# Kernel optimization log

Hardware: AMD Instinct MI355X
Metric: run time of the kernel (lower is better)

Reference implementation:

```python
import jax, jax.numpy as jnp
import numpy as np

DIM = 768
HEADS = 12
HEAD_DIM = DIM // HEADS


def setup_inputs() -> dict:
    key = jax.random.key(0)
    ks = jax.random.split(key, 5)
    B, N = 2, 2048
    x = jax.random.normal(ks[0], (B, N, DIM), dtype=jnp.float32)
    s = 1.0 / np.sqrt(DIM)
    qkv_w = jax.random.normal(ks[1], (3 * DIM, DIM), dtype=jnp.float32) * s
    qkv_b = jnp.zeros((3 * DIM,), dtype=jnp.float32)
    proj_w = jax.random.normal(ks[2], (DIM, DIM), dtype=jnp.float32) * s
    proj_b = jnp.zeros((DIM,), dtype=jnp.float32)
    return {"x": x, "qkv_w": qkv_w, "qkv_b": qkv_b, "proj_w": proj_w, "proj_b": proj_b}


def reference(x, qkv_w, qkv_b, proj_w, proj_b):
    B, N, C = x.shape
    scale = HEAD_DIM ** -0.5
    qkv = x @ qkv_w.T + qkv_b                      # [B,N,3C]
    qkv = qkv.reshape(B, N, 3, HEADS, HEAD_DIM)
    q = qkv[:, :, 0].transpose(0, 2, 1, 3)         # [B,H,N,D]
    k = qkv[:, :, 1].transpose(0, 2, 1, 3)
    v = qkv[:, :, 2].transpose(0, 2, 1, 3)
    attn = jnp.einsum('bhnd,bhmd->bhnm', q, k) * scale
    attn = jax.nn.softmax(attn, axis=-1)
    out = jnp.einsum('bhnm,bhmd->bhnd', attn, v)   # [B,H,N,D]
    out = out.transpose(0, 2, 1, 3).reshape(B, N, C)
    return out @ proj_w.T + proj_b
```

## Files before the change

kernel.cpp:

```cpp
#include <hip/hip_runtime.h>
#include <hip/hip_bf16.h>

typedef __bf16 bf16x8 __attribute__((ext_vector_type(8)));
typedef float f32x4 __attribute__((ext_vector_type(4)));
typedef float f32x16 __attribute__((ext_vector_type(16)));

#define SEQ   2048
#define NHEAD 12
#define NBH   24
#define QSCALE 0.18033688011112042f

__device__ __forceinline__ unsigned short f2bf(float f) {
  unsigned int u = __builtin_bit_cast(unsigned int, f);
  u += 0x7FFFu + ((u >> 16) & 1u);
  return (unsigned short)(u >> 16);
}
__device__ __forceinline__ unsigned int packbf2_trunc(float lo, float hi) {
  return __builtin_amdgcn_perm(__builtin_bit_cast(unsigned int, hi),
                               __builtin_bit_cast(unsigned int, lo), 0x07060302u);
}

#define NX4  786432
#define NW14 442368
#define NW24 147456
__global__ __launch_bounds__(256) void cvt3_kernel(const float4* __restrict__ x,
                                                   const float4* __restrict__ w1,
                                                   const float4* __restrict__ w2,
                                                   ushort4* __restrict__ xo,
                                                   ushort4* __restrict__ w1o,
                                                   ushort4* __restrict__ w2o) {
  int i = blockIdx.x * 256 + threadIdx.x;
  const float4* s;
  ushort4* d;
  int j = i;
  if (i < NX4)               { s = x;  d = xo; }
  else if (i < NX4 + NW14)   { s = w1; d = w1o; j = i - NX4; }
  else                       { s = w2; d = w2o; j = i - (NX4 + NW14); }
  float4 v = s[j];
  ushort4 r;
  r.x = f2bf(v.x); r.y = f2bf(v.y); r.z = f2bf(v.z); r.w = f2bf(v.w);
  d[j] = r;
}

template <int BM, int BN, int MODE>
__global__ __launch_bounds__(256) void gemm_kernel(const unsigned short* __restrict__ X,
                                                   const unsigned short* __restrict__ W,
                                                   const float* __restrict__ bias,
                                                   unsigned short* __restrict__ Qb,
                                                   unsigned short* __restrict__ Kb,
                                                   unsigned short* __restrict__ Vtb,
                                                   float* __restrict__ Out) {
  constexpr int K = 768, BK = 64;
  constexpr int WM = BM / 2, WN = BN / 2;
  constexpr int MT = WM / 16, NT = WN / 16;
  __shared__ __align__(16) unsigned short Xs[BM * BK];
  __shared__ __align__(16) unsigned short Ws[BN * BK];

  const int tid = threadIdx.x;
  const int w = tid >> 6, lane = tid & 63, quad = lane >> 4, m16 = lane & 15;
  const int wm = w & 1, wn = w >> 1;
  const int row0 = blockIdx.y * BM, col0 = blockIdx.x * BN;

  f32x4 acc[MT][NT];
#pragma unroll
  for (int mt = 0; mt < MT; ++mt)
#pragma unroll
    for (int nt = 0; nt < NT; ++nt) acc[mt][nt] = (f32x4){0.f, 0.f, 0.f, 0.f};

  for (int k0 = 0; k0 < K; k0 += BK) {
    __syncthreads();
#pragma unroll
    for (int j = 0; j < BM / 32; ++j) {
      int e = tid + 256 * j, r = e >> 3, c8 = e & 7;
      uint4 v = *(const uint4*)(X + (size_t)(row0 + r) * 768 + k0 + c8 * 8);
      *(uint4*)(Xs + r * BK + ((c8 ^ (r & 7)) << 3)) = v;
    }
#pragma unroll
    for (int j = 0; j < BN / 32; ++j) {
      int e = tid + 256 * j, r = e >> 3, c8 = e & 7;
      uint4 v = *(const uint4*)(W + (size_t)(col0 + r) * 768 + k0 + c8 * 8);
      *(uint4*)(Ws + r * BK + ((c8 ^ (r & 7)) << 3)) = v;
    }
    __syncthreads();
#pragma unroll
    for (int ks = 0; ks < 2; ++ks) {
      const int sw = ((quad + 4 * ks) ^ (m16 & 7)) << 3;
      bf16x8 a[MT], b[NT];
#pragma unroll
      for (int mt = 0; mt < MT; ++mt)
        a[mt] = *(const bf16x8*)(Xs + (wm * WM + mt * 16 + m16) * BK + sw);
#pragma unroll
      for (int nt = 0; nt < NT; ++nt)
        b[nt] = *(const bf16x8*)(Ws + (wn * WN + nt * 16 + m16) * BK + sw);
#pragma unroll
      for (int mt = 0; mt < MT; ++mt)
#pragma unroll
        for (int nt = 0; nt < NT; ++nt)
          acc[mt][nt] = __builtin_amdgcn_mfma_f32_16x16x32_bf16(a[mt], b[nt], acc[mt][nt], 0, 0, 0);
    }
  }

#pragma unroll
  for (int mt = 0; mt < MT; ++mt) {
#pragma unroll
    for (int nt = 0; nt < NT; ++nt) {
      const int m0 = row0 + wm * WM + mt * 16 + quad * 4;
      const int c = col0 + wn * WN + nt * 16 + m16;
      const float bia = bias[c];
      f32x4 v = acc[mt][nt];
      if constexpr (MODE == 0) {
        const int bidx = m0 >> 11, ns = m0 & 2047;
        if (c < 1536) {
          unsigned short* dst;
          float sc;
          int cc;
          if (c < 768) { cc = c; dst = Qb; sc = QSCALE; }
          else         { cc = c - 768; dst = Kb; sc = 1.0f; }
          const int h = cc >> 6, d = cc & 63;
          unsigned short* p = dst + ((size_t)(bidx * NHEAD + h) * SEQ + ns) * 64 + d;
          p[0]   = f2bf((v[0] + bia) * sc);
          p[64]  = f2bf((v[1] + bia) * sc);
          p[128] = f2bf((v[2] + bia) * sc);
          p[192] = f2bf((v[3] + bia) * sc);
        } else {
          const int cc = c - 1536, h = cc >> 6, d = cc & 63;
          ushort4 pk;
          pk.x = f2bf(v[0] + bia); pk.y = f2bf(v[1] + bia);
          pk.z = f2bf(v[2] + bia); pk.w = f2bf(v[3] + bia);
          *(ushort4*)(Vtb + ((size_t)(bidx * NHEAD + h) * 64 + d) * SEQ + ns) = pk;
        }
      } else {
        float* o = Out + (size_t)m0 * 768 + c;
        o[0]       = v[0] + bia;
        o[768]     = v[1] + bia;
        o[2 * 768] = v[2] + bia;
        o[3 * 768] = v[3] + bia;
      }
    }
  }
}

#define VPAD 136
__global__ __launch_bounds__(256, 2) void attn_kernel(const unsigned short* __restrict__ Qb,
                                                      const unsigned short* __restrict__ Kb,
                                                      const unsigned short* __restrict__ Vtb,
                                                      unsigned short* __restrict__ Ab) {
  __shared__ __align__(16) unsigned short Ks[128 * 64];
  __shared__ __align__(16) unsigned short Vts[64 * VPAD];

  const int tid = threadIdx.x;
  const int w = tid >> 6, lane = tid & 63, hi = lane >> 5, l32 = lane & 31;
  const int bh = blockIdx.x % NBH, qt = blockIdx.x / NBH;
  const int bb = bh / NHEAD, h = bh % NHEAD;
  const int q0 = qt * 128 + w * 32;

  const unsigned short* Qp = Qb + (size_t)bh * SEQ * 64;
  const unsigned short* Kp = Kb + (size_t)bh * SEQ * 64;
  const unsigned short* Vp = Vtb + (size_t)bh * 64 * SEQ;

  bf16x8 qf[4];
#pragma unroll
  for (int dc = 0; dc < 4; ++dc)
    qf[dc] = *(const bf16x8*)(Qp + (size_t)(q0 + l32) * 64 + dc * 16 + hi * 8);

  f32x16 o[2] = {};
  float m_i = -3.0e38f, l_i = 0.f;

  for (int kt = 0; kt < 16; ++kt) {
    __syncthreads();
#pragma unroll
    for (int j = 0; j < 4; ++j) {
      int e = tid + 256 * j, r = e >> 3, c8 = e & 7;
      uint4 v = *(const uint4*)(Kp + (size_t)(kt * 128 + r) * 64 + c8 * 8);
      *(uint4*)(Ks + r * 64 + ((c8 ^ (r & 7)) << 3)) = v;
    }
#pragma unroll
    for (int j = 0; j < 4; ++j) {
      int e = tid + 256 * j, d = e >> 4, c8 = e & 15;
      uint4 v = *(const uint4*)(Vp + (size_t)d * SEQ + kt * 128 + c8 * 8);
      unsigned short* row = Vts + d * VPAD + (c8 >> 1) * 16 + (c8 & 1) * 4;
      *(uint2*)(row)     = make_uint2(v.x, v.y);
      *(uint2*)(row + 8) = make_uint2(v.z, v.w);
    }
    __syncthreads();

    f32x16 st[4];
#pragma unroll
    for (int t32 = 0; t32 < 4; ++t32) {
      f32x16 s = {};
#pragma unroll
      for (int dc = 0; dc < 4; ++dc) {
        bf16x8 kf = *(const bf16x8*)(Ks + (t32 * 32 + l32) * 64 + ((((dc << 1) | hi) ^ (l32 & 7)) << 3));
        s = __builtin_amdgcn_mfma_f32_32x32x16_bf16(kf, qf[dc], s, 0, 0, 0);
      }
      st[t32] = s;
    }

    float tmax = st[0][0];
#pragma unroll
    for (int t32 = 0; t32 < 4; ++t32)
#pragma unroll
      for (int e = 0; e < 16; ++e) tmax = fmaxf(tmax, st[t32][e]);
    tmax = fmaxf(tmax, __shfl_xor(tmax, 32));
    const float mnew = fmaxf(m_i, tmax);
    const float alpha = exp2f(m_i - mnew);
    float ssum = 0.f;
    unsigned int pf[4][8];
#pragma unroll
    for (int t32 = 0; t32 < 4; ++t32) {
      float pv[16];
#pragma unroll
      for (int e = 0; e < 16; ++e) { pv[e] = exp2f(st[t32][e] - mnew); ssum += pv[e]; }
#pragma unroll
      for (int e2 = 0; e2 < 8; ++e2)
        pf[t32][e2] = packbf2_trunc(pv[2 * e2], pv[2 * e2 + 1]);
    }
    ssum += __shfl_xor(ssum, 32);
    l_i = l_i * alpha + ssum;
    m_i = mnew;
    o[0] *= alpha;
    o[1] *= alpha;

#pragma unroll
    for (int t32 = 0; t32 < 4; ++t32) {
#pragma unroll
      for (int hh = 0; hh < 2; ++hh) {
        bf16x8 pfrag = __builtin_bit_cast(bf16x8,
            make_uint4(pf[t32][hh * 4], pf[t32][hh * 4 + 1], pf[t32][hh * 4 + 2], pf[t32][hh * 4 + 3]));
        const int slotbase = t32 * 32 + hh * 16 + hi * 8;
#pragma unroll
        for (int dt = 0; dt < 2; ++dt) {
          bf16x8 vf = *(const bf16x8*)(Vts + (dt * 32 + l32) * VPAD + slotbase);
          o[dt] = __builtin_amdgcn_mfma_f32_32x32x16_bf16(vf, pfrag, o[dt], 0, 0, 0);
        }
      }
    }
  }

  const float rl = __builtin_amdgcn_rcpf(l_i);
  unsigned short* base = Ab + ((size_t)bb * SEQ + q0 + l32) * 768 + h * 64;
#pragma unroll
  for (int dt = 0; dt < 2; ++dt) {
#pragma unroll
    for (int run = 0; run < 4; ++run) {
      ushort4 pk;
      pk.x = f2bf(o[dt][run * 4 + 0] * rl);
      pk.y = f2bf(o[dt][run * 4 + 1] * rl);
      pk.z = f2bf(o[dt][run * 4 + 2] * rl);
      pk.w = f2bf(o[dt][run * 4 + 3] * rl);
      *(ushort4*)(base + dt * 32 + run * 8 + hi * 4) = pk;
    }
  }
}

extern "C" void kernel_launch(void* const* d_in, const int* in_sizes, int n_in,
                              void* d_out, int out_size, void* d_ws, size_t ws_size,
                              hipStream_t stream) {
  const float* x      = (const float*)d_in[0];
  const float* qkv_w  = (const float*)d_in[1];
  const float* qkv_b  = (const float*)d_in[2];
  const float* proj_w = (const float*)d_in[3];
  const float* proj_b = (const float*)d_in[4];
  float* out = (float*)d_out;

  unsigned short* xb  = (unsigned short*)d_ws;
  unsigned short* wqb = xb + 3145728;
  unsigned short* wpb = wqb + 1769472;
  unsigned short* Qb  = wpb + 589824;
  unsigned short* Kb  = Qb + 3145728;
  unsigned short* Vtb = Kb + 3145728;
  unsigned short* Ab  = Vtb + 3145728;

  cvt3_kernel<<<5376, 256, 0, stream>>>((const float4*)x, (const float4*)qkv_w, (const float4*)proj_w,
                                        (ushort4*)xb, (ushort4*)wqb, (ushort4*)wpb);
  gemm_kernel<128, 96, 0><<<dim3(24, 32), 256, 0, stream>>>(xb, wqb, qkv_b, Qb, Kb, Vtb, nullptr);
  attn_kernel<<<384, 256, 0, stream>>>(Qb, Kb, Vtb, Ab);
  gemm_kernel<64, 96, 1><<<dim3(8, 64), 256, 0, stream>>>(Ab, wpb, proj_b, nullptr, nullptr, nullptr, out);
}
```

Baseline: 178.4 us.

## Double-buffer attention K/V tiles with direct global-to-LDS loads and smaller blocks

The attention kernel now uses 128-thread blocks over 64-query tiles with 64-key tiles, double-buffered in LDS through global_load_lds so the next tile's copy overlaps the current tile's MFMA and softmax work. The GEMM staging also switches to direct global-to-LDS copies, with the XOR swizzle moved onto the source address. The V-transpose store permutes sequence positions so that V fragments match the P-fragment ordering without padding. Hardware exp2 intrinsics replace exp2f. The aim is to hide load latency and cut register round trips, at the cost of a single barrier per iteration and a finer grid.

```diff
diff --git a/kernel.cpp b/kernel.cpp
--- a/kernel.cpp
+++ b/kernel.cpp
@@ -10,6 +10,10 @@
 #define NBH   24
 #define QSCALE 0.18033688011112042f
 
+#define CP16(g, l) __builtin_amdgcn_global_load_lds( \
+    (const __attribute__((address_space(1))) unsigned int*)(g), \
+    (__attribute__((address_space(3))) unsigned int*)(l), 16, 0, 0)
+
 __device__ __forceinline__ unsigned short f2bf(float f) {
   unsigned int u = __builtin_bit_cast(unsigned int, f);
   u += 0x7FFFu + ((u >> 16) & 1u);
@@ -22,7 +26,6 @@
 
 #define NX4  786432
 #define NW14 442368
-#define NW24 147456
 __global__ __launch_bounds__(256) void cvt3_kernel(const float4* __restrict__ x,
                                                    const float4* __restrict__ w1,
                                                    const float4* __restrict__ w2,
@@ -72,14 +75,12 @@
 #pragma unroll
     for (int j = 0; j < BM / 32; ++j) {
       int e = tid + 256 * j, r = e >> 3, c8 = e & 7;
-      uint4 v = *(const uint4*)(X + (size_t)(row0 + r) * 768 + k0 + c8 * 8);
-      *(uint4*)(Xs + r * BK + ((c8 ^ (r & 7)) << 3)) = v;
+      CP16(X + (size_t)(row0 + r) * 768 + k0 + ((c8 ^ (r & 7)) << 3), Xs + e * 8);
     }
 #pragma unroll
     for (int j = 0; j < BN / 32; ++j) {
       int e = tid + 256 * j, r = e >> 3, c8 = e & 7;
-      uint4 v = *(const uint4*)(W + (size_t)(col0 + r) * 768 + k0 + c8 * 8);
-      *(uint4*)(Ws + r * BK + ((c8 ^ (r & 7)) << 3)) = v;
+      CP16(W + (size_t)(col0 + r) * 768 + k0 + ((c8 ^ (r & 7)) << 3), Ws + e * 8);
     }
     __syncthreads();
 #pragma unroll
@@ -124,10 +125,11 @@
           p[192] = f2bf((v[3] + bia) * sc);
         } else {
           const int cc = c - 1536, h = cc >> 6, d = cc & 63;
+          const int ns2 = (ns & ~12) | ((ns & 4) << 1) | ((ns & 8) >> 1);
           ushort4 pk;
           pk.x = f2bf(v[0] + bia); pk.y = f2bf(v[1] + bia);
           pk.z = f2bf(v[2] + bia); pk.w = f2bf(v[3] + bia);
-          *(ushort4*)(Vtb + ((size_t)(bidx * NHEAD + h) * 64 + d) * SEQ + ns) = pk;
+          *(ushort4*)(Vtb + ((size_t)(bidx * NHEAD + h) * 64 + d) * SEQ + ns2) = pk;
         }
       } else {
         float* o = Out + (size_t)m0 * 768 + c;
@@ -140,19 +142,18 @@
   }
 }
 
-#define VPAD 136
-__global__ __launch_bounds__(256, 2) void attn_kernel(const unsigned short* __restrict__ Qb,
-                                                      const unsigned short* __restrict__ Kb,
-                                                      const unsigned short* __restrict__ Vtb,
-                                                      unsigned short* __restrict__ Ab) {
-  __shared__ __align__(16) unsigned short Ks[128 * 64];
-  __shared__ __align__(16) unsigned short Vts[64 * VPAD];
+__global__ __launch_bounds__(128) void attn_kernel(const unsigned short* __restrict__ Qb,
+                                                   const unsigned short* __restrict__ Kb,
+                                                   const unsigned short* __restrict__ Vtb,
+                                                   unsigned short* __restrict__ Ab) {
+  __shared__ __align__(16) unsigned short Ks[2][64 * 64];
+  __shared__ __align__(16) unsigned short Vts[2][64 * 64];
 
   const int tid = threadIdx.x;
   const int w = tid >> 6, lane = tid & 63, hi = lane >> 5, l32 = lane & 31;
   const int bh = blockIdx.x % NBH, qt = blockIdx.x / NBH;
   const int bb = bh / NHEAD, h = bh % NHEAD;
-  const int q0 = qt * 128 + w * 32;
+  const int q0 = qt * 64 + w * 32;
 
   const unsigned short* Qp = Qb + (size_t)bh * SEQ * 64;
   const unsigned short* Kp = Kb + (size_t)bh * SEQ * 64;
@@ -163,54 +164,69 @@
   for (int dc = 0; dc < 4; ++dc)
     qf[dc] = *(const bf16x8*)(Qp + (size_t)(q0 + l32) * 64 + dc * 16 + hi * 8);
 
+#pragma unroll
+  for (int j = 0; j < 4; ++j) {
+    int e = tid + 128 * j, r = e >> 3, c8 = e & 7;
+    CP16(Kp + (size_t)r * 64 + ((c8 ^ (r & 7)) << 3), &Ks[0][e * 8]);
+    CP16(Vp + (size_t)r * SEQ + ((c8 ^ (r & 7)) << 3), &Vts[0][e * 8]);
+  }
+
   f32x16 o[2] = {};
   float m_i = -3.0e38f, l_i = 0.f;
 
-  for (int kt = 0; kt < 16; ++kt) {
+  for (int kt = 0; kt < 32; ++kt) {
+    const int cur = kt & 1;
     __syncthreads();
-#pragma unroll
-    for (int j = 0; j < 4; ++j) {
-      int e = tid + 256 * j, r = e >> 3, c8 = e & 7;
-      uint4 v = *(const uint4*)(Kp + (size_t)(kt * 128 + r) * 64 + c8 * 8);
-      *(uint4*)(Ks + r * 64 + ((c8 ^ (r & 7)) << 3)) = v;
-    }
-#pragma unroll
-    for (int j = 0; j < 4; ++j) {
-      int e = tid + 256 * j, d = e >> 4, c8 = e & 15;
-      uint4 v = *(const uint4*)(Vp + (size_t)d * SEQ + kt * 128 + c8 * 8);
-      unsigned short* row = Vts + d * VPAD + (c8 >> 1) * 16 + (c8 & 1) * 4;
-      *(uint2*)(row)     = make_uint2(v.x, v.y);
-      *(uint2*)(row + 8) = make_uint2(v.z, v.w);
-    }
-    __syncthreads();
-
-    f32x16 st[4];
-#pragma unroll
-    for (int t32 = 0; t32 < 4; ++t32) {
+
+    const unsigned short* Kc = Ks[cur];
+    const unsigned short* Vc = Vts[cur];
+    bf16x8 kf[2][4], vf[2][4];
+#pragma unroll
+    for (int t32 = 0; t32 < 2; ++t32)
+#pragma unroll
+      for (int dc = 0; dc < 4; ++dc)
+        kf[t32][dc] = *(const bf16x8*)(Kc + (t32 * 32 + l32) * 64 + ((((dc << 1) | hi) ^ (l32 & 7)) << 3));
+#pragma unroll
+    for (int dt = 0; dt < 2; ++dt)
+#pragma unroll
+      for (int cc = 0; cc < 4; ++cc)
+        vf[dt][cc] = *(const bf16x8*)(Vc + (dt * 32 + l32) * 64 + ((((cc << 1) | hi) ^ (l32 & 7)) << 3));
+
+    if (kt < 31) {
+      const int kn = kt + 1, nb = 1 - cur;
+#pragma unroll
+      for (int j = 0; j < 4; ++j) {
+        int e = tid + 128 * j, r = e >> 3, c8 = e & 7;
+        CP16(Kp + (size_t)(kn * 64 + r) * 64 + ((c8 ^ (r & 7)) << 3), &Ks[nb][e * 8]);
+        CP16(Vp + (size_t)r * SEQ + kn * 64 + ((c8 ^ (r & 7)) << 3), &Vts[nb][e * 8]);
+      }
+    }
+
+    f32x16 st[2];
+#pragma unroll
+    for (int t32 = 0; t32 < 2; ++t32) {
       f32x16 s = {};
 #pragma unroll
-      for (int dc = 0; dc < 4; ++dc) {
-        bf16x8 kf = *(const bf16x8*)(Ks + (t32 * 32 + l32) * 64 + ((((dc << 1) | hi) ^ (l32 & 7)) << 3));
-        s = __builtin_amdgcn_mfma_f32_32x32x16_bf16(kf, qf[dc], s, 0, 0, 0);
-      }
+      for (int dc = 0; dc < 4; ++dc)
+        s = __builtin_amdgcn_mfma_f32_32x32x16_bf16(kf[t32][dc], qf[dc], s, 0, 0, 0);
       st[t32] = s;
     }
 
     float tmax = st[0][0];
 #pragma unroll
-    for (int t32 = 0; t32 < 4; ++t32)
+    for (int t32 = 0; t32 < 2; ++t32)
 #pragma unroll
       for (int e = 0; e < 16; ++e) tmax = fmaxf(tmax, st[t32][e]);
     tmax = fmaxf(tmax, __shfl_xor(tmax, 32));
     const float mnew = fmaxf(m_i, tmax);
-    const float alpha = exp2f(m_i - mnew);
+    const float alpha = __builtin_amdgcn_exp2f(m_i - mnew);
     float ssum = 0.f;
-    unsigned int pf[4][8];
-#pragma unroll
-    for (int t32 = 0; t32 < 4; ++t32) {
+    unsigned int pf[2][8];
+#pragma unroll
+    for (int t32 = 0; t32 < 2; ++t32) {
       float pv[16];
 #pragma unroll
-      for (int e = 0; e < 16; ++e) { pv[e] = exp2f(st[t32][e] - mnew); ssum += pv[e]; }
+      for (int e = 0; e < 16; ++e) { pv[e] = __builtin_amdgcn_exp2f(st[t32][e] - mnew); ssum += pv[e]; }
 #pragma unroll
       for (int e2 = 0; e2 < 8; ++e2)
         pf[t32][e2] = packbf2_trunc(pv[2 * e2], pv[2 * e2 + 1]);
@@ -222,17 +238,15 @@
     o[1] *= alpha;
 
 #pragma unroll
-    for (int t32 = 0; t32 < 4; ++t32) {
+    for (int t32 = 0; t32 < 2; ++t32) {
 #pragma unroll
       for (int hh = 0; hh < 2; ++hh) {
         bf16x8 pfrag = __builtin_bit_cast(bf16x8,
             make_uint4(pf[t32][hh * 4], pf[t32][hh * 4 + 1], pf[t32][hh * 4 + 2], pf[t32][hh * 4 + 3]));
-        const int slotbase = t32 * 32 + hh * 16 + hi * 8;
-#pragma unroll
-        for (int dt = 0; dt < 2; ++dt) {
-          bf16x8 vf = *(const bf16x8*)(Vts + (dt * 32 + l32) * VPAD + slotbase);
-          o[dt] = __builtin_amdgcn_mfma_f32_32x32x16_bf16(vf, pfrag, o[dt], 0, 0, 0);
-        }
+        const int cc = 2 * t32 + hh;
+#pragma unroll
+        for (int dt = 0; dt < 2; ++dt)
+          o[dt] = __builtin_amdgcn_mfma_f32_32x32x16_bf16(vf[dt][cc], pfrag, o[dt], 0, 0, 0);
       }
     }
   }
@@ -274,6 +288,6 @@
   cvt3_kernel<<<5376, 256, 0, stream>>>((const float4*)x, (const float4*)qkv_w, (const float4*)proj_w,
                                         (ushort4*)xb, (ushort4*)wqb, (ushort4*)wpb);
   gemm_kernel<128, 96, 0><<<dim3(24, 32), 256, 0, stream>>>(xb, wqb, qkv_b, Qb, Kb, Vtb, nullptr);
-  attn_kernel<<<384, 256, 0, stream>>>(Qb, Kb, Vtb, Ab);
+  attn_kernel<<<768, 128, 0, stream>>>(Qb, Kb, Vtb, Ab);
   gemm_kernel<64, 96, 1><<<dim3(8, 64), 256, 0, stream>>>(Ab, wpb, proj_b, nullptr, nullptr, nullptr, out);
 }
```

After: 170.9 us. 4.2% less time.
